# Kernel optimization log

Hardware: AMD Instinct MI355X
Metric: run time of the kernel (lower is better)

The kernel has to match this reference:

```python
import jax, jax.numpy as jnp
import numpy as np
from jax import lax

T, B, D = 2048, 16, 1024


def setup_inputs() -> dict:
    key = jax.random.key(0)
    ks = jax.random.split(key, 3)
    xavier = (6.0 / (D + D)) ** 0.5  # xavier_uniform bound
    x = jax.random.normal(ks[0], (T, B, D), dtype=jnp.float32)
    W_alpha = jax.random.uniform(ks[1], (D, D), jnp.float32, -xavier, xavier)
    W_x = jax.random.uniform(ks[2], (D, D), jnp.float32, -xavier, xavier)
    b_alpha = jnp.full((D,), 2.0, jnp.float32)  # init_alpha_bias
    d_g = jnp.full((D,), 0.5, jnp.float32)      # init_d_g
    b_g = jnp.full((D,), 0.5, jnp.float32)      # init_b_g
    b_v = jnp.zeros((D,), jnp.float32)
    return {"x": x, "W_alpha": W_alpha, "b_alpha": b_alpha, "d_g": d_g,
            "b_g": b_g, "W_x": W_x, "b_v": b_v}


def reference(x, W_alpha, b_alpha, d_g, b_g, W_x, b_v):
    Tn, Bn, Dn = x.shape
    # Batched input projections (as in the torch code, done before the loop)
    alpha_all = jax.nn.sigmoid(jnp.einsum('tbd,ed->tbe', x, W_alpha) + b_alpha)  # [T,B,D]
    v_raw_all = jnp.tanh(jnp.einsum('tbd,ed->tbe', x, W_x) + b_v)                # [T,B,D]

    h0 = jnp.zeros((Bn, Dn), x.dtype)

    def step(h_prev, inp):
        alpha, v_raw = inp
        g = jax.nn.sigmoid(-d_g * jnp.abs(h_prev) + b_g)  # inverse self-gating
        v = v_raw * g
        h_new = alpha * h_prev + (1.0 - alpha) * v
        out = h_new * jax.nn.silu(h_new)
        return h_new, (h_new, out)

    _, (hs, outs) = lax.scan(step, h0, (alpha_all, v_raw_all))
    h = jnp.concatenate([h0[None], hs], axis=0)  # [T+1,B,D]
    return outs, h
```

## Files before the change

### kernel.cpp

```cpp
#include <hip/hip_runtime.h>
#include <hip/hip_fp16.h>

#define T_DIM 2048
#define B_DIM 16
#define D_DIM 1024
#define M_TOT (T_DIM * B_DIM)
#define N_TOT (2 * D_DIM)
#define K_TOT D_DIM
#define BD    (B_DIM * D_DIM)

typedef __attribute__((ext_vector_type(8))) short short8;
typedef __attribute__((ext_vector_type(4))) float floatx4;

__device__ __forceinline__ short f32_to_bf16(float f) {
  unsigned u = __float_as_uint(f);
  u = (u + 0x7FFFu + ((u >> 16) & 1u)) >> 16;
  return (short)u;
}

__global__ __launch_bounds__(256) void cast_bf16_k(const float* __restrict__ src,
                                                   short* __restrict__ dst) {
  const size_t i = ((size_t)blockIdx.x * 256 + threadIdx.x) * 8;
  floatx4 f0 = *(const floatx4*)(src + i);
  floatx4 f1 = *(const floatx4*)(src + i + 4);
  short8 o;
  o[0] = f32_to_bf16(f0[0]); o[1] = f32_to_bf16(f0[1]);
  o[2] = f32_to_bf16(f0[2]); o[3] = f32_to_bf16(f0[3]);
  o[4] = f32_to_bf16(f1[0]); o[5] = f32_to_bf16(f1[1]);
  o[6] = f32_to_bf16(f1[2]); o[7] = f32_to_bf16(f1[3]);
  *(short8*)(dst + i) = o;
}

#define GLDS16(gp, lp)                                                                   \
  __builtin_amdgcn_global_load_lds((const __attribute__((address_space(1))) void*)(gp),  \
                                   (__attribute__((address_space(3))) void*)(lp), 16, 0, 0)

__global__ __launch_bounds__(256, 2) void gemm_act_k(
    const short* __restrict__ xb, const short* __restrict__ wb,
    const float* __restrict__ b_alpha, const float* __restrict__ b_v,
    __half* __restrict__ pairbuf) {
  __shared__ __align__(16) short As[128 * 32];
  __shared__ __align__(16) short Bs[128 * 32];
  const int tid  = threadIdx.x;
  const int wave = tid >> 6;
  const int lane = tid & 63;
  const int quad = lane >> 4;
  const int l16  = lane & 15;
  const int mblk = blockIdx.y << 7;
  const int nblk = blockIdx.x << 7;
  const int wrow = (wave >> 1) << 6;
  const int wcol = (wave & 1) << 6;

  floatx4 acc[4][4];
#pragma unroll
  for (int i = 0; i < 4; ++i)
#pragma unroll
    for (int j = 0; j < 4; ++j) acc[i][j] = {0.f, 0.f, 0.f, 0.f};

  const int chunk_m = tid >> 2;
  const int c_swz   = (tid & 3) ^ (chunk_m & 3) ^ ((chunk_m >> 2) & 1);
  const short* gA0 = xb + (size_t)(mblk + chunk_m) * K_TOT + c_swz * 8;
  const short* gA1 = gA0 + (size_t)64 * K_TOT;
  const short* gB0 = wb + (size_t)(nblk + chunk_m) * K_TOT + c_swz * 8;
  const short* gB1 = gB0 + (size_t)64 * K_TOT;
  short* lA0 = As + wave * 512;
  short* lA1 = As + 2048 + wave * 512;
  short* lB0 = Bs + wave * 512;
  short* lB1 = Bs + 2048 + wave * 512;

  const int pl   = (l16 & 3) ^ ((l16 >> 2) & 1);
  const int aoff = (wrow + l16) * 32 + ((quad ^ pl) * 8);
  const int boff = (wcol + l16) * 32 + ((quad ^ pl) * 8);

  for (int k0 = 0; k0 < K_TOT; k0 += 32) {
    GLDS16(gA0 + k0, lA0);
    GLDS16(gA1 + k0, lA1);
    GLDS16(gB0 + k0, lB0);
    GLDS16(gB1 + k0, lB1);
    __syncthreads();
    short8 af[4], bf[4];
#pragma unroll
    for (int i = 0; i < 4; ++i) af[i] = *(const short8*)(As + aoff + i * 512);
#pragma unroll
    for (int i = 0; i < 4; ++i) bf[i] = *(const short8*)(Bs + boff + i * 512);
#pragma unroll
    for (int i = 0; i < 4; ++i)
#pragma unroll
      for (int j = 0; j < 4; ++j)
        acc[i][j] = __builtin_amdgcn_mfma_f32_16x16x32_bf16(af[i], bf[j], acc[i][j], 0, 0, 0);
    __syncthreads();
  }

  const bool isA = (nblk < D_DIM);
  const float* __restrict__ bias = isA ? b_alpha : b_v;
  const int hsel = isA ? 0 : 1;
#pragma unroll
  for (int j = 0; j < 4; ++j) {
    const int n_g = nblk + wcol + j * 16 + l16;
    const int e = isA ? n_g : (n_g - D_DIM);
    const float bz = bias[e];
#pragma unroll
    for (int i = 0; i < 4; ++i) {
      const floatx4 v = acc[i][j];
      const int m_base = mblk + wrow + i * 16 + quad * 4;
#pragma unroll
      for (int r = 0; r < 4; ++r) {
        const float z = v[r] + bz;
        float val;
        if (isA) {
          val = __builtin_amdgcn_rcpf(1.f + __expf(-z));
        } else {
          val = 1.f - 2.f * __builtin_amdgcn_rcpf(__expf(2.f * z) + 1.f);
        }
        pairbuf[((size_t)(m_base + r) * D_DIM + e) * 2 + hsel] = __float2half(val);
      }
    }
  }
}

__global__ __launch_bounds__(64) void scan_k(const __half2* __restrict__ pair,
                                             const float* __restrict__ d_g,
                                             const float* __restrict__ b_g,
                                             __half* __restrict__ hh) {
  const int c = blockIdx.x * 64 + threadIdx.x;
  const float LOG2E = 1.44269504f;
  const float dg = d_g[c & (D_DIM - 1)] * LOG2E;
  const float bg = b_g[c & (D_DIM - 1)] * LOG2E;
  hh[c] = __float2half(0.f);
  float h = 0.f;
  size_t idx = c;
  __half2 p[16];
#pragma unroll
  for (int k = 0; k < 16; ++k) p[k] = pair[idx + (size_t)k * BD];
  for (int t = 0; t < T_DIM; t += 16) {
    const size_t pfadd = (t + 16 < T_DIM) ? (size_t)16 * BD : 0;
#pragma unroll
    for (int k = 0; k < 16; ++k) {
      const float2 av = __half22float2(p[k]);
      p[k] = pair[idx + pfadd];
      const float w = (1.f - av.x) * av.y;
      const float e = __builtin_amdgcn_exp2f(fmaf(dg, fabsf(h), -bg));
      const float g = __builtin_amdgcn_rcpf(1.f + e);
      h = fmaf(av.x, h, w * g);
      hh[idx + BD] = __float2half(h);
      idx += BD;
    }
  }
}

__global__ __launch_bounds__(256) void silu_k(const __half* __restrict__ hh,
                                              float* __restrict__ outbuf) {
  const float LOG2E = 1.44269504f;
  const size_t i = ((size_t)blockIdx.x * 256 + threadIdx.x) * 8;
  float* __restrict__ outs = outbuf;
  float* __restrict__ hout = outbuf + (size_t)T_DIM * BD;
  const __half2* hp = (const __half2*)(hh + i);
  float hf[8];
#pragma unroll
  for (int j = 0; j < 4; ++j) {
    const float2 f = __half22float2(hp[j]);
    hf[2 * j] = f.x; hf[2 * j + 1] = f.y;
  }
  *(floatx4*)(hout + i)     = floatx4{hf[0], hf[1], hf[2], hf[3]};
  *(floatx4*)(hout + i + 4) = floatx4{hf[4], hf[5], hf[6], hf[7]};
  if (i >= BD) {
    float o[8];
#pragma unroll
    for (int j = 0; j < 8; ++j) {
      const float s = __builtin_amdgcn_rcpf(1.f + __builtin_amdgcn_exp2f(-LOG2E * hf[j]));
      o[j] = hf[j] * hf[j] * s;
    }
    *(floatx4*)(outs + i - BD)     = floatx4{o[0], o[1], o[2], o[3]};
    *(floatx4*)(outs + i - BD + 4) = floatx4{o[4], o[5], o[6], o[7]};
  }
}

extern "C" void kernel_launch(void* const* d_in, const int* in_sizes, int n_in,
                              void* d_out, int out_size, void* d_ws, size_t ws_size,
                              hipStream_t stream) {
  const float* x       = (const float*)d_in[0];
  const float* W_alpha = (const float*)d_in[1];
  const float* b_alpha = (const float*)d_in[2];
  const float* d_g     = (const float*)d_in[3];
  const float* b_g     = (const float*)d_in[4];
  const float* W_x     = (const float*)d_in[5];
  const float* b_v     = (const float*)d_in[6];
  float* out = (float*)d_out;

  char* ws = (char*)d_ws;
  short*  xb      = (short*)ws;
  short*  wb      = (short*)(ws + (size_t)67108864);
  __half* pairbuf = (__half*)(ws + (size_t)71303168);
  __half* h_half  = (__half*)ws;

  cast_bf16_k<<<M_TOT * K_TOT / (8 * 256), 256, 0, stream>>>(x, xb);
  cast_bf16_k<<<D_DIM * K_TOT / (8 * 256), 256, 0, stream>>>(W_alpha, wb);
  cast_bf16_k<<<D_DIM * K_TOT / (8 * 256), 256, 0, stream>>>(W_x, wb + (size_t)D_DIM * K_TOT);
  gemm_act_k<<<dim3(N_TOT / 128, M_TOT / 128), 256, 0, stream>>>(xb, wb, b_alpha, b_v, pairbuf);
  scan_k<<<BD / 64, 64, 0, stream>>>((const __half2*)pairbuf, d_g, b_g, h_half);
  silu_k<<<(T_DIM + 1) * BD / (8 * 256), 256, 0, stream>>>(h_half, out);
}
```

Baseline: 668.6 us.

## Fuse SiLU output computation into the scan kernel and drop the fp16 h buffer

The separate silu pass is removed. The scan kernel now computes out = h*silu(h) inline and writes both outputs straight to the fp32 output buffer. Loads are restructured into double-buffered blocks of 16 timesteps so the next block is prefetched while the current one is computed. This removes the intermediate fp16 h write/read round trip and one kernel launch. In exchange, the latency-bound scan (only 256 blocks of 64 threads) now carries the extra exp/rcp work and the larger fp32 stores.

```diff
diff --git a/kernel.cpp b/kernel.cpp
--- a/kernel.cpp
+++ b/kernel.cpp
@@ -118,60 +118,53 @@
   }
 }
 
-__global__ __launch_bounds__(64) void scan_k(const __half2* __restrict__ pair,
-                                             const float* __restrict__ d_g,
-                                             const float* __restrict__ b_g,
-                                             __half* __restrict__ hh) {
+__global__ __launch_bounds__(64) void scan_fused_k(const __half2* __restrict__ pair,
+                                                   const float* __restrict__ d_g,
+                                                   const float* __restrict__ b_g,
+                                                   float* __restrict__ outbuf) {
   const int c = blockIdx.x * 64 + threadIdx.x;
   const float LOG2E = 1.44269504f;
   const float dg = d_g[c & (D_DIM - 1)] * LOG2E;
   const float bg = b_g[c & (D_DIM - 1)] * LOG2E;
-  hh[c] = __float2half(0.f);
+  float* __restrict__ outs = outbuf;
+  float* __restrict__ hout = outbuf + (size_t)T_DIM * BD;
+  hout[c] = 0.f;
   float h = 0.f;
-  size_t idx = c;
-  __half2 p[16];
+
+  __half2 pc[16], pn[16];
 #pragma unroll
-  for (int k = 0; k < 16; ++k) p[k] = pair[idx + (size_t)k * BD];
+  for (int k = 0; k < 16; ++k) pc[k] = pair[(size_t)k * BD + c];
+
+  size_t sidx = c;
   for (int t = 0; t < T_DIM; t += 16) {
-    const size_t pfadd = (t + 16 < T_DIM) ? (size_t)16 * BD : 0;
+    const bool more = (t + 16 < T_DIM);
+    const size_t lbase = more ? ((size_t)(t + 16) * BD + c) : (size_t)c;
+    const size_t lstep = more ? (size_t)BD : 0;
+#pragma unroll
+    for (int k = 0; k < 16; ++k) pn[k] = pair[lbase + (size_t)k * lstep];
+
+    float hv[16], ov[16];
 #pragma unroll
     for (int k = 0; k < 16; ++k) {
-      const float2 av = __half22float2(p[k]);
-      p[k] = pair[idx + pfadd];
+      const float2 av = __half22float2(pc[k]);
       const float w = (1.f - av.x) * av.y;
       const float e = __builtin_amdgcn_exp2f(fmaf(dg, fabsf(h), -bg));
       const float g = __builtin_amdgcn_rcpf(1.f + e);
       h = fmaf(av.x, h, w * g);
-      hh[idx + BD] = __float2half(h);
-      idx += BD;
+      hv[k] = h;
+      const float s = __builtin_amdgcn_rcpf(1.f + __builtin_amdgcn_exp2f(-LOG2E * h));
+      ov[k] = h * (h * s);
     }
-  }
-}
 
-__global__ __launch_bounds__(256) void silu_k(const __half* __restrict__ hh,
-                                              float* __restrict__ outbuf) {
-  const float LOG2E = 1.44269504f;
-  const size_t i = ((size_t)blockIdx.x * 256 + threadIdx.x) * 8;
-  float* __restrict__ outs = outbuf;
-  float* __restrict__ hout = outbuf + (size_t)T_DIM * BD;
-  const __half2* hp = (const __half2*)(hh + i);
-  float hf[8];
 #pragma unroll
-  for (int j = 0; j < 4; ++j) {
-    const float2 f = __half22float2(hp[j]);
-    hf[2 * j] = f.x; hf[2 * j + 1] = f.y;
-  }
-  *(floatx4*)(hout + i)     = floatx4{hf[0], hf[1], hf[2], hf[3]};
-  *(floatx4*)(hout + i + 4) = floatx4{hf[4], hf[5], hf[6], hf[7]};
-  if (i >= BD) {
-    float o[8];
+    for (int k = 0; k < 16; ++k) {
+      outs[sidx + (size_t)k * BD] = ov[k];
+      hout[sidx + (size_t)k * BD + BD] = hv[k];
+    }
+    sidx += (size_t)16 * BD;
+
 #pragma unroll
-    for (int j = 0; j < 8; ++j) {
-      const float s = __builtin_amdgcn_rcpf(1.f + __builtin_amdgcn_exp2f(-LOG2E * hf[j]));
-      o[j] = hf[j] * hf[j] * s;
-    }
-    *(floatx4*)(outs + i - BD)     = floatx4{o[0], o[1], o[2], o[3]};
-    *(floatx4*)(outs + i - BD + 4) = floatx4{o[4], o[5], o[6], o[7]};
+    for (int k = 0; k < 16; ++k) pc[k] = pn[k];
   }
 }
 
@@ -191,12 +184,10 @@
   short*  xb      = (short*)ws;
   short*  wb      = (short*)(ws + (size_t)67108864);
   __half* pairbuf = (__half*)(ws + (size_t)71303168);
-  __half* h_half  = (__half*)ws;
 
   cast_bf16_k<<<M_TOT * K_TOT / (8 * 256), 256, 0, stream>>>(x, xb);
   cast_bf16_k<<<D_DIM * K_TOT / (8 * 256), 256, 0, stream>>>(W_alpha, wb);
   cast_bf16_k<<<D_DIM * K_TOT / (8 * 256), 256, 0, stream>>>(W_x, wb + (size_t)D_DIM * K_TOT);
   gemm_act_k<<<dim3(N_TOT / 128, M_TOT / 128), 256, 0, stream>>>(xb, wb, b_alpha, b_v, pairbuf);
-  scan_k<<<BD / 64, 64, 0, stream>>>((const __half2*)pairbuf, d_g, b_g, h_half);
-  silu_k<<<(T_DIM + 1) * BD / (8 * 256), 256, 0, stream>>>(h_half, out);
+  scan_fused_k<<<BD / 64, 64, 0, stream>>>((const __half2*)pairbuf, d_g, b_g, out);
 }
```

After: 687.3 us. 2.8% more time.

## Use 256x256 multi-stage pipelined GEMM tiles and deeper scan prefetch

Applied to the files above, without the earlier changes.

The GEMM moves to 256x256 tiles with 8 waves and a 4-stage LDS ring filled by direct global-to-LDS loads, using explicit vmcnt waits and raw barriers so loads overlap MFMA work. MFMA priority is raised while computing. The scan kernel now prefetches pair data 32 steps ahead with double-buffered register chunks to hide memory latency in the serial recurrence. The larger LDS footprint (128KB) limits occupancy to one block per CU and raises register pressure.

```diff
diff --git a/kernel.cpp b/kernel.cpp
--- a/kernel.cpp
+++ b/kernel.cpp
@@ -35,60 +35,81 @@
   __builtin_amdgcn_global_load_lds((const __attribute__((address_space(1))) void*)(gp),  \
                                    (__attribute__((address_space(3))) void*)(lp), 16, 0, 0)
 
-__global__ __launch_bounds__(256, 2) void gemm_act_k(
+__global__ __launch_bounds__(512, 2) void gemm_act_k(
     const short* __restrict__ xb, const short* __restrict__ wb,
     const float* __restrict__ b_alpha, const float* __restrict__ b_v,
     __half* __restrict__ pairbuf) {
-  __shared__ __align__(16) short As[128 * 32];
-  __shared__ __align__(16) short Bs[128 * 32];
+  __shared__ __align__(16) short smem[65536];
   const int tid  = threadIdx.x;
   const int wave = tid >> 6;
   const int lane = tid & 63;
   const int quad = lane >> 4;
   const int l16  = lane & 15;
-  const int mblk = blockIdx.y << 7;
-  const int nblk = blockIdx.x << 7;
-  const int wrow = (wave >> 1) << 6;
-  const int wcol = (wave & 1) << 6;
-
-  floatx4 acc[4][4];
-#pragma unroll
-  for (int i = 0; i < 4; ++i)
+  const int wm   = wave >> 2;
+  const int wn   = wave & 3;
+  const int nblk = blockIdx.x << 8;
+  const int mblk = blockIdx.y << 8;
+
+  floatx4 acc[8][4];
+#pragma unroll
+  for (int i = 0; i < 8; ++i)
 #pragma unroll
     for (int j = 0; j < 4; ++j) acc[i][j] = {0.f, 0.f, 0.f, 0.f};
 
-  const int chunk_m = tid >> 2;
-  const int c_swz   = (tid & 3) ^ (chunk_m & 3) ^ ((chunk_m >> 2) & 1);
-  const short* gA0 = xb + (size_t)(mblk + chunk_m) * K_TOT + c_swz * 8;
-  const short* gA1 = gA0 + (size_t)64 * K_TOT;
-  const short* gB0 = wb + (size_t)(nblk + chunk_m) * K_TOT + c_swz * 8;
-  const short* gB1 = gB0 + (size_t)64 * K_TOT;
-  short* lA0 = As + wave * 512;
-  short* lA1 = As + 2048 + wave * 512;
-  short* lB0 = Bs + wave * 512;
-  short* lB1 = Bs + 2048 + wave * 512;
+  const int rowA  = tid >> 2;
+  const int c_swz = (tid & 3) ^ (rowA & 3) ^ ((rowA >> 2) & 1);
+  const short* gA0 = xb + (size_t)(mblk + rowA) * K_TOT + c_swz * 8;
+  const short* gA1 = gA0 + (size_t)128 * K_TOT;
+  const short* gB0 = wb + (size_t)(nblk + rowA) * K_TOT + c_swz * 8;
+  const short* gB1 = gB0 + (size_t)128 * K_TOT;
+
+#define STAGE(s_, k0_) do {                                   \
+    short* aA = smem + (s_) * 8192 + wave * 512;              \
+    short* aB = smem + 32768 + (s_) * 8192 + wave * 512;      \
+    GLDS16(gA0 + (k0_), aA);                                  \
+    GLDS16(gA1 + (k0_), aA + 4096);                           \
+    GLDS16(gB0 + (k0_), aB);                                  \
+    GLDS16(gB1 + (k0_), aB + 4096);                           \
+  } while (0)
 
   const int pl   = (l16 & 3) ^ ((l16 >> 2) & 1);
-  const int aoff = (wrow + l16) * 32 + ((quad ^ pl) * 8);
-  const int boff = (wcol + l16) * 32 + ((quad ^ pl) * 8);
-
-  for (int k0 = 0; k0 < K_TOT; k0 += 32) {
-    GLDS16(gA0 + k0, lA0);
-    GLDS16(gA1 + k0, lA1);
-    GLDS16(gB0 + k0, lB0);
-    GLDS16(gB1 + k0, lB1);
-    __syncthreads();
-    short8 af[4], bf[4];
-#pragma unroll
-    for (int i = 0; i < 4; ++i) af[i] = *(const short8*)(As + aoff + i * 512);
-#pragma unroll
-    for (int i = 0; i < 4; ++i) bf[i] = *(const short8*)(Bs + boff + i * 512);
-#pragma unroll
-    for (int i = 0; i < 4; ++i)
+  const int aoff = (wm * 128 + l16) * 32 + ((quad ^ pl) * 8);
+  const int boff = 32768 + (wn * 64 + l16) * 32 + ((quad ^ pl) * 8);
+
+  STAGE(0, 0);
+  STAGE(1, 32);
+  STAGE(2, 64);
+  asm volatile("s_waitcnt vmcnt(8)" ::: "memory");
+  __builtin_amdgcn_sched_barrier(0);
+  __builtin_amdgcn_s_barrier();
+  __builtin_amdgcn_sched_barrier(0);
+
+  for (int t = 0; t < 32; ++t) {
+    const int s = t & 3;
+    const int k0n = (t < 29) ? (t + 3) * 32 : 0;
+    STAGE((t + 3) & 3, k0n);
+
+    const short* sb = smem + s * 8192;
+    short8 af[8], bf[4];
+#pragma unroll
+    for (int i = 0; i < 8; ++i) af[i] = *(const short8*)(sb + aoff + i * 512);
+#pragma unroll
+    for (int j = 0; j < 4; ++j) bf[j] = *(const short8*)(sb + boff + j * 512);
+
+    __builtin_amdgcn_s_setprio(1);
+#pragma unroll
+    for (int i = 0; i < 8; ++i)
 #pragma unroll
       for (int j = 0; j < 4; ++j)
         acc[i][j] = __builtin_amdgcn_mfma_f32_16x16x32_bf16(af[i], bf[j], acc[i][j], 0, 0, 0);
-    __syncthreads();
+    __builtin_amdgcn_s_setprio(0);
+
+    asm volatile("s_waitcnt lgkmcnt(0)" ::: "memory");
+    __builtin_amdgcn_sched_barrier(0);
+    asm volatile("s_waitcnt vmcnt(8)" ::: "memory");
+    __builtin_amdgcn_sched_barrier(0);
+    __builtin_amdgcn_s_barrier();
+    __builtin_amdgcn_sched_barrier(0);
   }
 
   const bool isA = (nblk < D_DIM);
@@ -96,13 +117,13 @@
   const int hsel = isA ? 0 : 1;
 #pragma unroll
   for (int j = 0; j < 4; ++j) {
-    const int n_g = nblk + wcol + j * 16 + l16;
+    const int n_g = nblk + wn * 64 + j * 16 + l16;
     const int e = isA ? n_g : (n_g - D_DIM);
     const float bz = bias[e];
 #pragma unroll
-    for (int i = 0; i < 4; ++i) {
+    for (int i = 0; i < 8; ++i) {
       const floatx4 v = acc[i][j];
-      const int m_base = mblk + wrow + i * 16 + quad * 4;
+      const int m_base = mblk + wm * 128 + i * 16 + quad * 4;
 #pragma unroll
       for (int r = 0; r < 4; ++r) {
         const float z = v[r] + bz;
@@ -116,6 +137,7 @@
       }
     }
   }
+#undef STAGE
 }
 
 __global__ __launch_bounds__(64) void scan_k(const __half2* __restrict__ pair,
@@ -128,23 +150,36 @@
   const float bg = b_g[c & (D_DIM - 1)] * LOG2E;
   hh[c] = __float2half(0.f);
   float h = 0.f;
-  size_t idx = c;
-  __half2 p[16];
-#pragma unroll
-  for (int k = 0; k < 16; ++k) p[k] = pair[idx + (size_t)k * BD];
+
+  __half2 pc[16], pn[16], pf[16];
+#pragma unroll
+  for (int k = 0; k < 16; ++k) pc[k] = pair[(size_t)k * BD + c];
+#pragma unroll
+  for (int k = 0; k < 16; ++k) pn[k] = pair[(size_t)(k + 16) * BD + c];
+
+  size_t sidx = c;
   for (int t = 0; t < T_DIM; t += 16) {
-    const size_t pfadd = (t + 16 < T_DIM) ? (size_t)16 * BD : 0;
+    const bool more = (t + 32 < T_DIM);
+    const size_t lbase = more ? ((size_t)(t + 32) * BD + c) : (size_t)c;
+    const size_t lstep = more ? (size_t)BD : 0;
+#pragma unroll
+    for (int k = 0; k < 16; ++k) pf[k] = pair[lbase + (size_t)k * lstep];
+
 #pragma unroll
     for (int k = 0; k < 16; ++k) {
-      const float2 av = __half22float2(p[k]);
-      p[k] = pair[idx + pfadd];
+      const float2 av = __half22float2(pc[k]);
       const float w = (1.f - av.x) * av.y;
       const float e = __builtin_amdgcn_exp2f(fmaf(dg, fabsf(h), -bg));
       const float g = __builtin_amdgcn_rcpf(1.f + e);
       h = fmaf(av.x, h, w * g);
-      hh[idx + BD] = __float2half(h);
-      idx += BD;
+      hh[sidx + (size_t)k * BD + BD] = __float2half(h);
     }
+    sidx += (size_t)16 * BD;
+
+#pragma unroll
+    for (int k = 0; k < 16; ++k) pc[k] = pn[k];
+#pragma unroll
+    for (int k = 0; k < 16; ++k) pn[k] = pf[k];
   }
 }
 
@@ -196,7 +231,7 @@
   cast_bf16_k<<<M_TOT * K_TOT / (8 * 256), 256, 0, stream>>>(x, xb);
   cast_bf16_k<<<D_DIM * K_TOT / (8 * 256), 256, 0, stream>>>(W_alpha, wb);
   cast_bf16_k<<<D_DIM * K_TOT / (8 * 256), 256, 0, stream>>>(W_x, wb + (size_t)D_DIM * K_TOT);
-  gemm_act_k<<<dim3(N_TOT / 128, M_TOT / 128), 256, 0, stream>>>(xb, wb, b_alpha, b_v, pairbuf);
+  gemm_act_k<<<dim3(N_TOT / 256, M_TOT / 256), 512, 0, stream>>>(xb, wb, b_alpha, b_v, pairbuf);
   scan_k<<<BD / 64, 64, 0, stream>>>((const __half2*)pairbuf, d_g, b_g, h_half);
   silu_k<<<(T_DIM + 1) * BD / (8 * 256), 256, 0, stream>>>(h_half, out);
 }
```

After: 684.5 us. +2.4%, slower.
